# Optimization experiments

Hardware: AMD Instinct MI355X
Metric: run time of the kernel (lower is better)

## Reference

```python
import jax, jax.numpy as jnp
import numpy as np

SEQ_LEN = 200
BATCH = 4096
V = 50000


def setup_inputs() -> dict:
    key = jax.random.key(0)
    k1, k2, k3 = jax.random.split(key, 3)
    text = jax.random.randint(k1, (SEQ_LEN, BATCH), 0, V, dtype=jnp.int64)
    W = jax.random.normal(k2, (1, V), dtype=jnp.float32)
    b = jax.random.normal(k3, (1,), dtype=jnp.float32)
    return {"text": text, "W": W, "b": b}


def reference(text, W, b):
    # text: [L, B] int token ids. Original builds word_vecs[phrase, val] += 1
    # iterating over Counter KEYS -> binary presence indicator per document.
    L, B = text.shape
    rows = jnp.arange(B)[:, None]                      # [B, 1]
    word_vecs = jnp.zeros((B, V), dtype=jnp.float32).at[rows, text.T].set(1.0)  # [B, V]
    # nn.Linear(V, 1): y = x @ W.T + b
    return word_vecs @ W.T + b                          # [B, 1]
```

## Files before the change

### kernel.cpp

```cpp
#include <hip/hip_runtime.h>

constexpr int SEQ_LEN = 200;
constexpr int BATCH   = 4096;
constexpr int V       = 50000;

constexpr int DOCS    = 16;
constexpr int NTHR    = 512;
constexpr int SLICES  = NTHR / DOCS;
constexpr int TOK_PT  = (SEQ_LEN + SLICES - 1) / SLICES;
constexpr int HSLOTS  = 512;
constexpr unsigned EMPTY = 0xFFFFFFFFu;

__global__ __launch_bounds__(NTHR) void MNB_8151847928093_kernel(
    const int*   __restrict__ text,
    const float* __restrict__ W,
    const float* __restrict__ bias,
    float*       __restrict__ out)
{
    __shared__ unsigned ht[HSLOTS * DOCS];
    __shared__ float    psum[SLICES * DOCS];

    const int tid   = threadIdx.x;
    const int doc   = tid & (DOCS - 1);
    const int slice = tid >> 4;
    const int b     = blockIdx.x * DOCS + doc;

    for (int i = tid; i < HSLOTS * DOCS; i += NTHR) ht[i] = EMPTY;
    __syncthreads();

    unsigned toks[TOK_PT];
    #pragma unroll
    for (int i = 0; i < TOK_PT; ++i) {
        const int t = slice + i * SLICES;
        toks[i] = (t < SEQ_LEN) ? (unsigned)text[t * BATCH + b] : EMPTY;
    }

    float sum = 0.0f;
    #pragma unroll
    for (int i = 0; i < TOK_PT; ++i) {
        const unsigned tok = toks[i];
        if (tok == EMPTY) continue;
        unsigned slot = ((tok * 2654435761u) >> 16) & (HSLOTS - 1);
        while (true) {
            const unsigned old = atomicCAS(&ht[slot * DOCS + doc], EMPTY, tok);
            if (old == EMPTY) { sum += W[tok]; break; }
            if (old == tok)   { break; }
            slot = (slot + 1) & (HSLOTS - 1);
        }
    }

    psum[slice * DOCS + doc] = sum;
    __syncthreads();

    if (tid < DOCS) {
        float s = bias[0];
        #pragma unroll
        for (int k = 0; k < SLICES; ++k) s += psum[k * DOCS + tid];
        out[blockIdx.x * DOCS + tid] = s;
    }
}

extern "C" void kernel_launch(void* const* d_in, const int* in_sizes, int n_in,
                              void* d_out, int out_size, void* d_ws, size_t ws_size,
                              hipStream_t stream) {
    const int*   text = (const int*)d_in[0];
    const float* W    = (const float*)d_in[1];
    const float* bias = (const float*)d_in[2];
    float*       out  = (float*)d_out;

    MNB_8151847928093_kernel<<<BATCH / DOCS, NTHR, 0, stream>>>(text, W, bias, out);
}
```

Measured before the change: 65.88 us.

## Prefetch W values speculatively, batch first-probe CAS, wave-shuffle reduce, 1024 threads

```diff
diff --git a/kernel.cpp b/kernel.cpp
--- a/kernel.cpp
+++ b/kernel.cpp
@@ -5,7 +5,7 @@
 constexpr int V       = 50000;
 
 constexpr int DOCS    = 16;
-constexpr int NTHR    = 512;
+constexpr int NTHR    = 1024;
 constexpr int SLICES  = NTHR / DOCS;
 constexpr int TOK_PT  = (SEQ_LEN + SLICES - 1) / SLICES;
 constexpr int HSLOTS  = 512;
@@ -18,7 +18,7 @@
     float*       __restrict__ out)
 {
     __shared__ unsigned ht[HSLOTS * DOCS];
-    __shared__ float    psum[SLICES * DOCS];
+    __shared__ float    psum[(NTHR / 64) * DOCS];
 
     const int tid   = threadIdx.x;
     const int doc   = tid & (DOCS - 1);
@@ -35,27 +35,49 @@
         toks[i] = (t < SEQ_LEN) ? (unsigned)text[t * BATCH + b] : EMPTY;
     }
 
+    float wv[TOK_PT];
+    #pragma unroll
+    for (int i = 0; i < TOK_PT; ++i)
+        wv[i] = W[toks[i] == EMPTY ? 0u : toks[i]];
+
+    unsigned hs[TOK_PT], od[TOK_PT];
+    #pragma unroll
+    for (int i = 0; i < TOK_PT; ++i) {
+        hs[i] = ((toks[i] * 2654435761u) >> 16) & (HSLOTS - 1);
+        od[i] = (toks[i] != EMPTY)
+                    ? atomicCAS(&ht[hs[i] * DOCS + doc], EMPTY, toks[i])
+                    : 0u;
+    }
+
     float sum = 0.0f;
     #pragma unroll
     for (int i = 0; i < TOK_PT; ++i) {
         const unsigned tok = toks[i];
         if (tok == EMPTY) continue;
-        unsigned slot = ((tok * 2654435761u) >> 16) & (HSLOTS - 1);
-        while (true) {
-            const unsigned old = atomicCAS(&ht[slot * DOCS + doc], EMPTY, tok);
-            if (old == EMPTY) { sum += W[tok]; break; }
-            if (old == tok)   { break; }
-            slot = (slot + 1) & (HSLOTS - 1);
+        const unsigned old = od[i];
+        if (old == EMPTY) { sum += wv[i]; }
+        else if (old != tok) {
+            unsigned slot = (hs[i] + 1) & (HSLOTS - 1);
+            while (true) {
+                const unsigned o = atomicCAS(&ht[slot * DOCS + doc], EMPTY, tok);
+                if (o == EMPTY) { sum += wv[i]; break; }
+                if (o == tok)   { break; }
+                slot = (slot + 1) & (HSLOTS - 1);
+            }
         }
     }
 
-    psum[slice * DOCS + doc] = sum;
+    sum += __shfl_down(sum, 32, 64);
+    sum += __shfl_down(sum, 16, 64);
+    const int wave = tid >> 6;
+    const int lane = tid & 63;
+    if (lane < DOCS) psum[wave * DOCS + lane] = sum;
     __syncthreads();
 
     if (tid < DOCS) {
         float s = bias[0];
         #pragma unroll
-        for (int k = 0; k < SLICES; ++k) s += psum[k * DOCS + tid];
+        for (int k = 0; k < NTHR / 64; ++k) s += psum[k * DOCS + tid];
         out[blockIdx.x * DOCS + tid] = s;
     }
 }
```

Result: faster. 63.95 us (-2.9%).
